# Kernel tuning notes

Hardware: AMD Instinct MI355X
Metric: run time of the kernel (lower is better)

The kernel has to match this reference:

```python
import jax, jax.numpy as jnp
import numpy as np

D_MODEL = 1024
HEADS = 16
D_K = D_MODEL // HEADS
PB_DIM = D_MODEL // 4  # 256, ContinuousPositionBias hidden dim
LEAKY_SLOPE = 0.01     # nn.LeakyReLU default


def setup_inputs() -> dict:
    key = jax.random.key(0)
    ks = jax.random.split(key, 16)
    B, S = 4, 1024

    def lin_w(k, fan_in, fan_out):
        # stored as [in, out]; y = x @ W + b  (equivalent math to torch Linear)
        return (jax.random.normal(k, (fan_in, fan_out), jnp.float32)
                / np.float32(np.sqrt(fan_in)))

    inp = {
        "query": jax.random.normal(ks[0], (B, S, D_MODEL), jnp.float32),
        "key":   jax.random.normal(ks[1], (B, S, D_MODEL), jnp.float32),
        "value": jax.random.normal(ks[2], (B, S, D_MODEL), jnp.float32),
        "wq": lin_w(ks[3], D_MODEL, D_MODEL), "bq": jnp.zeros((D_MODEL,), jnp.float32),
        "wk": lin_w(ks[4], D_MODEL, D_MODEL), "bk": jnp.zeros((D_MODEL,), jnp.float32),
        "wv": lin_w(ks[5], D_MODEL, D_MODEL), "bv": jnp.zeros((D_MODEL,), jnp.float32),
        "wo": lin_w(ks[6], D_MODEL, D_MODEL), "bo": jnp.zeros((D_MODEL,), jnp.float32),
        # ContinuousPositionBias MLP: Linear(2,dim)+LeakyReLU -> Linear(dim,dim)+LeakyReLU -> Linear(dim,heads)
        "pb_w0": lin_w(ks[7], 2, PB_DIM),      "pb_b0": jnp.zeros((PB_DIM,), jnp.float32),
        "pb_w1": lin_w(ks[8], PB_DIM, PB_DIM), "pb_b1": jnp.zeros((PB_DIM,), jnp.float32),
        "pb_w2": lin_w(ks[9], PB_DIM, HEADS),  "pb_b2": jnp.zeros((HEADS,), jnp.float32),
        "patch_height": 32,
        "patch_width": 32,
    }
    return inp


def _pos_bias(pb_w0, pb_b0, pb_w1, pb_b1, pb_w2, pb_b2, h, w):
    gy, gx = jnp.meshgrid(jnp.arange(h), jnp.arange(w), indexing="ij")
    pos = jnp.stack([gy, gx], axis=-1).reshape(-1, 2).astype(jnp.float32)  # [n, 2]
    rel = pos[:, None, :] - pos[None, :, :]                                # [n, n, 2]
    x = jax.nn.leaky_relu(rel @ pb_w0 + pb_b0, LEAKY_SLOPE)
    x = jax.nn.leaky_relu(x @ pb_w1 + pb_b1, LEAKY_SLOPE)
    x = x @ pb_w2 + pb_b2                                                  # [n, n, H]
    return jnp.transpose(x, (2, 0, 1))                                     # [H, n, n]


def reference(query, key, value, wq, bq, wk, bk, wv, bv, wo, bo,
              pb_w0, pb_b0, pb_w1, pb_b1, pb_w2, pb_b2,
              patch_height, patch_width):
    B, S, D = query.shape
    split = lambda x: x.reshape(B, S, HEADS, D_K).transpose(0, 2, 1, 3)  # [B,H,S,d]
    Q = split(query @ wq + bq)
    K = split(key @ wk + bk)
    V = split(value @ wv + bv)

    scores = jnp.einsum("bhqd,bhkd->bhqk", Q, K) / np.float32(np.sqrt(D_K))
    bias = _pos_bias(pb_w0, pb_b0, pb_w1, pb_b1, pb_w2, pb_b2,
                     patch_height, patch_width)                          # [H,S,S]
    scores = scores + bias[None]

    attn = jax.nn.softmax(scores, axis=-1)  # dropout is identity at inference
    ctx = jnp.einsum("bhqk,bhkd->bhqd", attn, V)
    ctx = ctx.transpose(0, 2, 1, 3).reshape(B, S, D)
    return ctx @ wo + bo
```

## Files before the change

### kernel.cpp

```cpp
#include <hip/hip_runtime.h>
#include <stdint.h>

typedef unsigned short u16;
typedef unsigned int   u32;
typedef __attribute__((ext_vector_type(4))) float f32x4;
typedef __attribute__((ext_vector_type(8))) short s16x8;
typedef __attribute__((ext_vector_type(2))) u32 u32x2;

__device__ __forceinline__ u16 f2bf(float f) {
  u32 u = __builtin_bit_cast(u32, f);
  u = (u + 0x7FFFu + ((u >> 16) & 1u)) >> 16;
  return (u16)u;
}

__device__ __forceinline__ u32 cvt_pk_bf16(float lo, float hi) {
  u32 r;
  asm("v_cvt_pk_bf16_f32 %0, %1, %2" : "=v"(r) : "v"(lo), "v"(hi));
  return r;
}

__device__ __forceinline__ void gload_lds16(const void* g, void* l) {
  __builtin_amdgcn_global_load_lds((const __attribute__((address_space(1))) void*)g,
                                   (__attribute__((address_space(3))) void*)l,
                                   16, 0, 0);
}

#define MFMA16(a, b, c) __builtin_amdgcn_mfma_f32_16x16x32_bf16((a), (b), (c), 0, 0, 0)

__global__ void k_cast(const float* __restrict__ q, const float* __restrict__ k,
                       const float* __restrict__ v,
                       u16* __restrict__ oq, u16* __restrict__ ok, u16* __restrict__ ov) {
  const int z = blockIdx.z;
  const float* src = (z == 0) ? q : (z == 1) ? k : v;
  u16* dst = (z == 0) ? oq : (z == 1) ? ok : ov;
  const int i = (blockIdx.x * 256 + threadIdx.x) * 4;
  const float4 f = *(const float4*)(src + i);
  ushort4 o4;
  o4.x = f2bf(f.x); o4.y = f2bf(f.y); o4.z = f2bf(f.z); o4.w = f2bf(f.w);
  *(ushort4*)(dst + i) = o4;
}

__global__ void k_transpose_w(const float* __restrict__ w0, const float* __restrict__ w1,
                              const float* __restrict__ w2, const float* __restrict__ w3,
                              u16* __restrict__ o0, u16* __restrict__ o1,
                              u16* __restrict__ o2, u16* __restrict__ o3) {
  __shared__ float t[64][65];
  const int z = blockIdx.z;
  const float* w = (z == 0) ? w0 : (z == 1) ? w1 : (z == 2) ? w2 : w3;
  u16* o = (z == 0) ? o0 : (z == 1) ? o1 : (z == 2) ? o2 : o3;
  const int k0 = blockIdx.x * 64;
  const int n0 = blockIdx.y * 64;
  const int tx = threadIdx.x & 63, ty = threadIdx.x >> 6;
#pragma unroll
  for (int i = 0; i < 16; ++i) {
    const int r = ty * 16 + i;
    t[r][tx] = w[(size_t)(k0 + r) * 1024 + n0 + tx];
  }
  __syncthreads();
#pragma unroll
  for (int i = 0; i < 16; ++i) {
    const int r = ty * 16 + i;
    o[(size_t)(n0 + r) * 1024 + k0 + tx] = f2bf(t[tx][r]);
  }
}

__global__ __launch_bounds__(256) void k_posbias(
    const float* __restrict__ w0, const float* __restrict__ b0,
    const float* __restrict__ w1, const float* __restrict__ b1,
    const float* __restrict__ w2, const float* __restrict__ b2,
    float* __restrict__ tbl) {
  __shared__ float h0[4][264];
  __shared__ float h1[4][264];
  __shared__ float pr[4][4][16];
  const int t = threadIdx.x;
  const int p0 = blockIdx.x * 4;
  {
    const float wy = w0[t], wx = w0[256 + t], bb = b0[t];
#pragma unroll
    for (int r = 0; r < 4; ++r) {
      int p = p0 + r; if (p > 3968) p = 3968;
      const float dy = (float)(p / 63 - 31);
      const float dx = (float)(p % 63 - 31);
      const float v = dy * wy + dx * wx + bb;
      h0[r][t] = v > 0.f ? v : 0.01f * v;
    }
  }
  __syncthreads();
  {
    const float bb = b1[t];
    float a0 = bb, a1 = bb, a2 = bb, a3 = bb;
    for (int k = 0; k < 256; k += 4) {
      const float wA = w1[(k + 0) * 256 + t];
      const float wB = w1[(k + 1) * 256 + t];
      const float wC = w1[(k + 2) * 256 + t];
      const float wD = w1[(k + 3) * 256 + t];
      const float4 x0 = *(const float4*)&h0[0][k];
      const float4 x1 = *(const float4*)&h0[1][k];
      const float4 x2 = *(const float4*)&h0[2][k];
      const float4 x3 = *(const float4*)&h0[3][k];
      a0 += (x0.x * wA + x0.y * wB) + (x0.z * wC + x0.w * wD);
      a1 += (x1.x * wA + x1.y * wB) + (x1.z * wC + x1.w * wD);
      a2 += (x2.x * wA + x2.y * wB) + (x2.z * wC + x2.w * wD);
      a3 += (x3.x * wA + x3.y * wB) + (x3.z * wC + x3.w * wD);
    }
    h1[0][t] = a0 > 0.f ? a0 : 0.01f * a0;
    h1[1][t] = a1 > 0.f ? a1 : 0.01f * a1;
    h1[2][t] = a2 > 0.f ? a2 : 0.01f * a2;
    h1[3][t] = a3 > 0.f ? a3 : 0.01f * a3;
  }
  __syncthreads();
  {
    const int hh = t & 15, r = (t >> 4) & 3, q = t >> 6;
    const int k0 = q * 64;
    float acc = 0.f;
    for (int k = k0; k < k0 + 64; ++k)
      acc += h1[r][k] * w2[k * 16 + hh];
    pr[q][r][hh] = acc;
  }
  __syncthreads();
  if (t < 64) {
    const int hh = t & 15, r = t >> 4;
    const int p = p0 + r;
    if (p < 3969)
      tbl[hh * 3969 + p] =
          b2[hh] + ((pr[0][r][hh] + pr[1][r][hh]) + (pr[2][r][hh] + pr[3][r][hh]));
  }
}

template <int MODE>
__global__ __launch_bounds__(512, 4) void k_gemm(
    const u16* __restrict__ A0, const u16* __restrict__ A1, const u16* __restrict__ A2,
    const u16* __restrict__ B0, const u16* __restrict__ B1, const u16* __restrict__ B2,
    const float* __restrict__ c0, const float* __restrict__ c1, const float* __restrict__ c2,
    void* __restrict__ o0, void* __restrict__ o1, void* __restrict__ o2,
    int Mdim, int Ndim, int Kdim) {
  __shared__ u16 sA[2][128 * 64];
  __shared__ u16 sB[2][128 * 64];

  const int nxy = gridDim.x * gridDim.y;
  const int nwg = nxy * gridDim.z;
  int wg = blockIdx.x + gridDim.x * blockIdx.y + nxy * blockIdx.z;
  wg = (wg & 7) * (nwg >> 3) + (wg >> 3);
  const int z = wg / nxy;
  const int rem = wg % nxy;
  const int by = rem / gridDim.x;
  const int bx = rem % gridDim.x;

  const u16* A  = (z == 0) ? A0 : (z == 1) ? A1 : A2;
  const u16* Bt = (z == 0) ? B0 : (z == 1) ? B1 : B2;
  const float* bias = (z == 0) ? c0 : (z == 1) ? c1 : c2;

  const int tid = threadIdx.x, lane = tid & 63, w = tid >> 6;
  const int wr = w & 3, wc = w >> 2;
  const int m0 = by * 128, n0 = bx * 128;

  const int srow = tid >> 3, sslot = tid & 7;
  const int scol = (sslot ^ (srow & 7)) * 8;
  const u16* aBase = A  + (size_t)(m0 + srow) * Kdim + scol;
  const u16* bBase = Bt + (size_t)(n0 + srow) * Kdim + scol;

  const int qlo = lane & 15, g = lane >> 4;
  const int swz = (qlo & 7) << 3;

#define GSTAGE(buf, kt_)                                                         \
  {                                                                              \
    _Pragma("unroll")                                                            \
    for (int i_ = 0; i_ < 2; ++i_) {                                             \
      gload_lds16(aBase + (size_t)(i_ * 64) * Kdim + (kt_),                      \
                  &sA[buf][(i_ * 64 + srow) * 64 + sslot * 8]);                  \
      gload_lds16(bBase + (size_t)(i_ * 64) * Kdim + (kt_),                      \
                  &sB[buf][(i_ * 64 + srow) * 64 + sslot * 8]);                  \
    }                                                                            \
  }

  f32x4 acc[2][4] = {};

  GSTAGE(0, 0);
  __syncthreads();

  int cur = 0;
  for (int kt = 0; kt < Kdim; kt += 64) {
    if (kt + 64 < Kdim) GSTAGE(cur ^ 1, kt + 64);
    __builtin_amdgcn_s_setprio(1);
#pragma unroll
    for (int ks = 0; ks < 2; ++ks) {
      s16x8 af[2], bf[4];
#pragma unroll
      for (int m = 0; m < 2; ++m)
        af[m] = *(const s16x8*)(&sA[cur][(wr * 32 + m * 16 + qlo) * 64 + ((ks * 32 + g * 8) ^ swz)]);
#pragma unroll
      for (int n = 0; n < 4; ++n)
        bf[n] = *(const s16x8*)(&sB[cur][(wc * 64 + n * 16 + qlo) * 64 + ((ks * 32 + g * 8) ^ swz)]);
#pragma unroll
      for (int m = 0; m < 2; ++m)
#pragma unroll
        for (int n = 0; n < 4; ++n)
          acc[m][n] = MFMA16(af[m], bf[n], acc[m][n]);
    }
    __builtin_amdgcn_s_setprio(0);
    __syncthreads();
    cur ^= 1;
  }
#undef GSTAGE

  if (MODE == 0) {
    u16* out = (u16*)((z == 0) ? o0 : (z == 1) ? o1 : o2);
#pragma unroll
    for (int m = 0; m < 2; ++m) {
      const int gm = m0 + wr * 32 + m * 16 + (g << 2);
#pragma unroll
      for (int n = 0; n < 4; ++n) {
        const int gn = n0 + wc * 64 + n * 16 + qlo;
        const float bv = bias[gn];
        const int hh = gn >> 6, dd = gn & 63;
#pragma unroll
        for (int r = 0; r < 4; ++r) {
          const int row = gm + r;
          const int batch = row >> 10, ss = row & 1023;
          out[(((size_t)(batch * 16 + hh)) * 1024 + ss) * 64 + dd] = f2bf(acc[m][n][r] + bv);
        }
      }
    }
  } else {
    float* out = (float*)o0;
#pragma unroll
    for (int m = 0; m < 2; ++m) {
      const int gm = m0 + wr * 32 + m * 16 + (g << 2);
#pragma unroll
      for (int n = 0; n < 4; ++n) {
        const int gn = n0 + wc * 64 + n * 16 + qlo;
        const float bv = bias[gn];
#pragma unroll
        for (int r = 0; r < 4; ++r)
          out[(size_t)(gm + r) * Ndim + gn] = acc[m][n][r] + bv;
      }
    }
  }
}

__global__ void k_vt(const u16* __restrict__ Vb, u16* __restrict__ Vt) {
  __shared__ u32 t[64][65];
  const int bh = blockIdx.y, s0 = blockIdx.x * 64;
  const int tx = threadIdx.x & 63, ty = threadIdx.x >> 6;
  const u16* src = Vb + (size_t)bh * 65536;
  u16* dst = Vt + (size_t)bh * 65536;
#pragma unroll
  for (int i = 0; i < 16; ++i) {
    const int r = ty * 16 + i;
    t[r][tx] = src[(size_t)(s0 + r) * 64 + tx];
  }
  __syncthreads();
#pragma unroll
  for (int i = 0; i < 16; ++i) {
    const int r = ty * 16 + i;
    dst[(size_t)r * 1024 + s0 + tx] = (u16)t[tx][r];
  }
}

__global__ __launch_bounds__(256, 2) void k_attn(
    const u16* __restrict__ Qb,
    const u16* __restrict__ Kb,
    const u16* __restrict__ Vt,
    const float* __restrict__ tbl,
    u16* __restrict__ ctx) {
  __shared__ u16 sK[2][64 * 64];
  __shared__ u16 sV[2][64 * 64];
  __shared__ u32 sP[4][2][16][32];
  __shared__ float sTw[2205];

  const int f = blockIdx.x;
  const int nid = (f & 7) * 64 + (f >> 3);
  const int bh = nid >> 3, qblk = nid & 7;
  const int h = bh & 15, b = bh >> 4;
  const int q0 = qblk * 128, yq0 = qblk * 4;

  const int tid = threadIdx.x, lane = tid & 63, w = tid >> 6;
  const int qlo = lane & 15, g = lane >> 4;
  const u16* Qp = Qb + (size_t)bh * (1024 * 64);
  const u16* Kp = Kb + (size_t)bh * (1024 * 64);
  const u16* Vp = Vt + (size_t)bh * (64 * 1024);

  const int srow = lane >> 3, sslot = lane & 7;
  const int scol = ((sslot ^ srow) * 8);
  const int swz = (qlo & 7) << 3;

#define STAGE(buf, kv0_)                                                          \
  {                                                                               \
    _Pragma("unroll")                                                             \
    for (int i_ = 0; i_ < 2; ++i_) {                                              \
      const int row_ = w * 16 + i_ * 8 + srow;                                    \
      gload_lds16(Kp + (size_t)((kv0_) + row_) * 64 + scol,                       \
                  &sK[buf][row_ * 64 + sslot * 8]);                               \
      gload_lds16(Vp + (size_t)row_ * 1024 + (kv0_) + scol,                       \
                  &sV[buf][row_ * 64 + sslot * 8]);                               \
    }                                                                             \
  }

  STAGE(0, 0);

  {
    const float* tblh = tbl + h * 3969 + yq0 * 63;
    for (int i = tid; i < 2205; i += 256) sTw[i] = tblh[i];
  }

  s16x8 qf[2][2];
  int W2i[2];
#pragma unroll
  for (int m = 0; m < 2; ++m) {
    const int qi = q0 + w * 32 + m * 16 + qlo;
#pragma unroll
    for (int ks = 0; ks < 2; ++ks)
      qf[m][ks] = *(const s16x8*)(Qp + (size_t)qi * 64 + ks * 32 + g * 8);
    W2i[m] = (w + 31) * 63 + (m * 16 + qlo) + 31 - g * 4;
  }

  f32x4 accO[2][4] = {};
  float mrow[2] = {-3e38f, -3e38f}, lrow[2] = {0.f, 0.f};

  __syncthreads();

  int cur = 0;
  for (int t = 0; t < 16; ++t) {
    const int kv0 = t * 64;
    if (t != 15) STAGE(cur ^ 1, kv0 + 64);

    f32x4 sc[2][4] = {};
    __builtin_amdgcn_s_setprio(1);
#pragma unroll
    for (int ks = 0; ks < 2; ++ks) {
      s16x8 kf[4];
#pragma unroll
      for (int n = 0; n < 4; ++n)
        kf[n] = *(const s16x8*)(&sK[cur][(n * 16 + qlo) * 64 + ((ks * 32 + g * 8) ^ swz)]);
#pragma unroll
      for (int m = 0; m < 2; ++m)
#pragma unroll
        for (int n = 0; n < 4; ++n)
          sc[m][n] = MFMA16(kf[n], qf[m][ks], sc[m][n]);
    }
    __builtin_amdgcn_s_setprio(0);

    const int bk = (kv0 >> 5) * 63;
#pragma unroll
    for (int m = 0; m < 2; ++m) {
      const int bofs = W2i[m] - bk;
      float sv[16], mx = -3e38f;
#pragma unroll
      for (int n = 0; n < 4; ++n)
#pragma unroll
        for (int r = 0; r < 4; ++r) {
          const float val = sc[m][n][r] * 0.125f +
                            sTw[bofs - ((n >> 1) * 63 + (n & 1) * 16 + r)];
          sv[n * 4 + r] = val;
          mx = fmaxf(mx, val);
        }
      mx = fmaxf(mx, __shfl_xor(mx, 16));
      mx = fmaxf(mx, __shfl_xor(mx, 32));
      const float mold = mrow[m];
      const float mnew = fmaxf(mold, mx);
      const float alpha = __expf(mold - mnew);
      mrow[m] = mnew;
      float p[16], rs = 0.f;
#pragma unroll
      for (int i = 0; i < 16; ++i) { p[i] = __expf(sv[i] - mnew); rs += p[i]; }
      rs += __shfl_xor(rs, 16);
      rs += __shfl_xor(rs, 32);
      lrow[m] = lrow[m] * alpha + rs;
#pragma unroll
      for (int n = 0; n < 4; ++n) accO[m][n] *= alpha;

      u32* const prow = &sP[w][m][qlo][0];
      const int dswz = (qlo & 7) << 2;
#pragma unroll
      for (int n = 0; n < 4; ++n) {
        u32x2 pk;
        pk.x = cvt_pk_bf16(p[n * 4 + 0], p[n * 4 + 1]);
        pk.y = cvt_pk_bf16(p[n * 4 + 2], p[n * 4 + 3]);
        *(u32x2*)&prow[(n * 8 + g * 2) ^ dswz] = pk;
      }
    }

    __builtin_amdgcn_s_setprio(1);
#pragma unroll
    for (int ks = 0; ks < 2; ++ks) {
      s16x8 av[4];
#pragma unroll
      for (int n = 0; n < 4; ++n)
        av[n] = *(const s16x8*)(&sV[cur][(n * 16 + qlo) * 64 + ((ks * 32 + g * 8) ^ swz)]);
#pragma unroll
      for (int m = 0; m < 2; ++m) {
        const u16* myPm = (const u16*)&sP[w][m][0][0];
        const s16x8 pf = *(const s16x8*)(myPm + qlo * 64 + ((ks * 32 + g * 8) ^ swz));
#pragma unroll
        for (int n = 0; n < 4; ++n)
          accO[m][n] = MFMA16(av[n], pf, accO[m][n]);
      }
    }
    __builtin_amdgcn_s_setprio(0);

    __syncthreads();
    cur ^= 1;
  }

#pragma unroll
  for (int m = 0; m < 2; ++m) {
    const float inv = 1.0f / lrow[m];
    const int qi = q0 + w * 32 + m * 16 + qlo;
#pragma unroll
    for (int n = 0; n < 4; ++n) {
      ushort4 o4;
      o4.x = f2bf(accO[m][n][0] * inv);
      o4.y = f2bf(accO[m][n][1] * inv);
      o4.z = f2bf(accO[m][n][2] * inv);
      o4.w = f2bf(accO[m][n][3] * inv);
      *(ushort4*)(ctx + ((size_t)(b * 1024 + qi)) * 1024 + h * 64 + n * 16 + g * 4) = o4;
    }
  }
#undef STAGE
}

extern "C" void kernel_launch(void* const* d_in, const int* in_sizes, int n_in,
                              void* d_out, int out_size, void* d_ws, size_t ws_size,
                              hipStream_t stream) {
  const float* query = (const float*)d_in[0];
  const float* key   = (const float*)d_in[1];
  const float* value = (const float*)d_in[2];
  const float* wq = (const float*)d_in[3];
  const float* bq = (const float*)d_in[4];
  const float* wk = (const float*)d_in[5];
  const float* bk = (const float*)d_in[6];
  const float* wv = (const float*)d_in[7];
  const float* bv = (const float*)d_in[8];
  const float* wo = (const float*)d_in[9];
  const float* bo = (const float*)d_in[10];
  const float* pw0 = (const float*)d_in[11];
  const float* pb0 = (const float*)d_in[12];
  const float* pw1 = (const float*)d_in[13];
  const float* pb1 = (const float*)d_in[14];
  const float* pw2 = (const float*)d_in[15];
  const float* pb2 = (const float*)d_in[16];

  char* ws = (char*)d_ws;
  u16* Xq  = (u16*)(ws + 0);
  u16* Xk  = (u16*)(ws + 8388608);
  u16* Xv  = (u16*)(ws + 16777216);
  u16* Wtq = (u16*)(ws + 25165824);
  u16* Wtk = (u16*)(ws + 27262976);
  u16* Wtv = (u16*)(ws + 29360128);
  u16* Wto = (u16*)(ws + 31457280);
  u16* Qb  = (u16*)(ws + 33554432);
  u16* Kb  = (u16*)(ws + 41943040);
  u16* Vb  = (u16*)(ws + 50331648);
  u16* Vtb = (u16*)(ws + 58720256);
  u16* ctx = (u16*)(ws + 67108864);
  float* tbl = (float*)(ws + 75497472);

  k_cast<<<dim3(4096, 1, 3), 256, 0, stream>>>(query, key, value, Xq, Xk, Xv);
  k_transpose_w<<<dim3(16, 16, 4), 256, 0, stream>>>(wq, wk, wv, wo, Wtq, Wtk, Wtv, Wto);
  k_posbias<<<dim3(993), 256, 0, stream>>>(pw0, pb0, pw1, pb1, pw2, pb2, tbl);
  k_gemm<0><<<dim3(8, 32, 3), 512, 0, stream>>>(Xq, Xk, Xv, Wtq, Wtk, Wtv,
                                                bq, bk, bv, Qb, Kb, Vb, 4096, 1024, 1024);
  k_vt<<<dim3(16, 64), 256, 0, stream>>>(Vb, Vtb);
  k_attn<<<dim3(512), 256, 0, stream>>>(Qb, Kb, Vtb, tbl, ctx);
  k_gemm<1><<<dim3(8, 32, 1), 512, 0, stream>>>(ctx, ctx, ctx, Wto, Wto, Wto,
                                                bo, bo, bo, d_out, d_out, d_out, 4096, 1024, 1024);
}
```

Before: 143.0 us.

## Replace online softmax max tracking with precomputed per-query bias max offset

Adds a small kernel that computes, per head and query position, the maximum positional bias over all keys, using a separable sliding-window max over the bias table. The attention kernel then uses that fixed value as the softmax offset instead of a running max. This removes the per-tile max reduction, the cross-lane shuffles, the alpha rescaling of the accumulators and the running-sum rescale. The bias table is prescaled by 1/ln2 so a raw v_exp_f32 can be used. The risk is numerical: the offset ignores the QK term, so large attention scores could overflow or underflow exp2. It also adds one extra kernel launch.

```diff
diff --git a/kernel.cpp b/kernel.cpp
--- a/kernel.cpp
+++ b/kernel.cpp
@@ -19,6 +19,12 @@
   return r;
 }
 
+__device__ __forceinline__ float exp2_f(float x) {
+  float r;
+  asm("v_exp_f32 %0, %1" : "=v"(r) : "v"(x));
+  return r;
+}
+
 __device__ __forceinline__ void gload_lds16(const void* g, void* l) {
   __builtin_amdgcn_global_load_lds((const __attribute__((address_space(1))) void*)g,
                                    (__attribute__((address_space(3))) void*)l,
@@ -26,6 +32,9 @@
 }
 
 #define MFMA16(a, b, c) __builtin_amdgcn_mfma_f32_16x16x32_bf16((a), (b), (c), 0, 0, 0)
+
+#define INVLN2 1.44269504f
+#define SC_X_INVLN2 0.18033688f
 
 __global__ void k_cast(const float* __restrict__ q, const float* __restrict__ k,
                        const float* __restrict__ v,
@@ -123,7 +132,30 @@
     const int p = p0 + r;
     if (p < 3969)
       tbl[hh * 3969 + p] =
-          b2[hh] + ((pr[0][r][hh] + pr[1][r][hh]) + (pr[2][r][hh] + pr[3][r][hh]));
+          (b2[hh] + ((pr[0][r][hh] + pr[1][r][hh]) + (pr[2][r][hh] + pr[3][r][hh]))) * INVLN2;
+  }
+}
+
+__global__ void k_wmax(const float* __restrict__ tbl, float* __restrict__ M2) {
+  __shared__ float T[3969];
+  __shared__ float R[63 * 32];
+  const int h = blockIdx.x, tid = threadIdx.x;
+  for (int i = tid; i < 3969; i += 256) T[i] = tbl[h * 3969 + i];
+  __syncthreads();
+  for (int idx = tid; idx < 63 * 32; idx += 256) {
+    const int dy = idx >> 5, xq = idx & 31;
+    float m = -3e38f;
+#pragma unroll
+    for (int j = 0; j < 32; ++j) m = fmaxf(m, T[dy * 63 + xq + j]);
+    R[idx] = m;
+  }
+  __syncthreads();
+  for (int idx = tid; idx < 1024; idx += 256) {
+    const int yq = idx >> 5, xq = idx & 31;
+    float m = -3e38f;
+#pragma unroll
+    for (int j = 0; j < 32; ++j) m = fmaxf(m, R[(yq + j) * 32 + xq]);
+    M2[h * 1024 + idx] = m;
   }
 }
 
@@ -262,6 +294,7 @@
     const u16* __restrict__ Kb,
     const u16* __restrict__ Vt,
     const float* __restrict__ tbl,
+    const float* __restrict__ M2,
     u16* __restrict__ ctx) {
   __shared__ u16 sK[2][64 * 64];
   __shared__ u16 sV[2][64 * 64];
@@ -305,6 +338,7 @@
 
   s16x8 qf[2][2];
   int W2i[2];
+  float Mq[2];
 #pragma unroll
   for (int m = 0; m < 2; ++m) {
     const int qi = q0 + w * 32 + m * 16 + qlo;
@@ -312,10 +346,11 @@
     for (int ks = 0; ks < 2; ++ks)
       qf[m][ks] = *(const s16x8*)(Qp + (size_t)qi * 64 + ks * 32 + g * 8);
     W2i[m] = (w + 31) * 63 + (m * 16 + qlo) + 31 - g * 4;
+    Mq[m] = M2[h * 1024 + (yq0 + w) * 32 + (m * 16 + qlo)];
   }
 
   f32x4 accO[2][4] = {};
-  float mrow[2] = {-3e38f, -3e38f}, lrow[2] = {0.f, 0.f};
+  float lp[2] = {0.f, 0.f};
 
   __syncthreads();
 
@@ -344,30 +379,16 @@
 #pragma unroll
     for (int m = 0; m < 2; ++m) {
       const int bofs = W2i[m] - bk;
-      float sv[16], mx = -3e38f;
+      const float mq = Mq[m];
+      float p[16];
 #pragma unroll
       for (int n = 0; n < 4; ++n)
 #pragma unroll
-        for (int r = 0; r < 4; ++r) {
-          const float val = sc[m][n][r] * 0.125f +
-                            sTw[bofs - ((n >> 1) * 63 + (n & 1) * 16 + r)];
-          sv[n * 4 + r] = val;
-          mx = fmaxf(mx, val);
-        }
-      mx = fmaxf(mx, __shfl_xor(mx, 16));
-      mx = fmaxf(mx, __shfl_xor(mx, 32));
-      const float mold = mrow[m];
-      const float mnew = fmaxf(mold, mx);
-      const float alpha = __expf(mold - mnew);
-      mrow[m] = mnew;
-      float p[16], rs = 0.f;
-#pragma unroll
-      for (int i = 0; i < 16; ++i) { p[i] = __expf(sv[i] - mnew); rs += p[i]; }
-      rs += __shfl_xor(rs, 16);
-      rs += __shfl_xor(rs, 32);
-      lrow[m] = lrow[m] * alpha + rs;
-#pragma unroll
-      for (int n = 0; n < 4; ++n) accO[m][n] *= alpha;
+        for (int r = 0; r < 4; ++r)
+          p[n * 4 + r] = exp2_f(sc[m][n][r] * SC_X_INVLN2 +
+                                (sTw[bofs - ((n >> 1) * 63 + (n & 1) * 16 + r)] - mq));
+      lp[m] += (((p[0] + p[1]) + (p[2] + p[3])) + ((p[4] + p[5]) + (p[6] + p[7]))) +
+               (((p[8] + p[9]) + (p[10] + p[11])) + ((p[12] + p[13]) + (p[14] + p[15])));
 
       u32* const prow = &sP[w][m][qlo][0];
       const int dswz = (qlo & 7) << 2;
@@ -404,7 +425,10 @@
 
 #pragma unroll
   for (int m = 0; m < 2; ++m) {
-    const float inv = 1.0f / lrow[m];
+    float rs = lp[m];
+    rs += __shfl_xor(rs, 16);
+    rs += __shfl_xor(rs, 32);
+    const float inv = 1.0f / rs;
     const int qi = q0 + w * 32 + m * 16 + qlo;
 #pragma unroll
     for (int n = 0; n < 4; ++n) {
@@ -454,14 +478,16 @@
   u16* Vtb = (u16*)(ws + 58720256);
   u16* ctx = (u16*)(ws + 67108864);
   float* tbl = (float*)(ws + 75497472);
+  float* M2  = (float*)(ws + 75759616);
 
   k_cast<<<dim3(4096, 1, 3), 256, 0, stream>>>(query, key, value, Xq, Xk, Xv);
   k_transpose_w<<<dim3(16, 16, 4), 256, 0, stream>>>(wq, wk, wv, wo, Wtq, Wtk, Wtv, Wto);
   k_posbias<<<dim3(993), 256, 0, stream>>>(pw0, pb0, pw1, pb1, pw2, pb2, tbl);
+  k_wmax<<<dim3(16), 256, 0, stream>>>(tbl, M2);
   k_gemm<0><<<dim3(8, 32, 3), 512, 0, stream>>>(Xq, Xk, Xv, Wtq, Wtk, Wtv,
                                                 bq, bk, bv, Qb, Kb, Vb, 4096, 1024, 1024);
   k_vt<<<dim3(16, 64), 256, 0, stream>>>(Vb, Vtb);
-  k_attn<<<dim3(512), 256, 0, stream>>>(Qb, Kb, Vtb, tbl, ctx);
+  k_attn<<<dim3(512), 256, 0, stream>>>(Qb, Kb, Vtb, tbl, M2, ctx);
   k_gemm<1><<<dim3(8, 32, 1), 512, 0, stream>>>(ctx, ctx, ctx, Wto, Wto, Wto,
                                                 bo, bo, bo, d_out, d_out, d_out, 4096, 1024, 1024);
 }
```

Measured after the change: 144.1 us. About the same (+0.7%).
